# Optimization experiments

Measured on AMD Instinct MI355X. Metric: run time of the kernel, lower is better.

The kernel has to match this reference:

```python
import jax, jax.numpy as jnp
import numpy as np


def setup_inputs() -> dict:
    key = jax.random.key(0)
    k1, k2 = jax.random.split(key)
    N, I, J, K = 256, 32, 32, 256
    x = jax.random.normal(k1, (N, I, K), dtype=jnp.float32)
    z = jax.random.normal(k2, (N, J, K), dtype=jnp.float32)
    return {"x": x, "z": z}


def reference(x, z):
    # Original torch code loops over batch rolls; rolling only permutes the set
    # over which log_softmax (a permutation-invariant logsumexp) is taken, and
    # index 0 of the roll stack is always the diagonal pair (x[n], z[n]).
    # So it is exactly a symmetric InfoNCE over the full pairwise score matrix.
    J = z.shape[1]
    # Full pairwise token-level similarity: [N_x, N_z, I, J]
    sim = jnp.einsum('aik,bjk->abij', x, z)
    # score(x_a, z_b) = sum_{i,j} softmax_i(sim)*sim / J
    w = jax.nn.softmax(sim, axis=2) * sim
    S = w.sum(axis=(2, 3)) / J  # [N_x, N_z]
    diag = jnp.diagonal(S)
    # loss_x[n] = -log_softmax over x-candidates (axis 0) at the diagonal
    loss_x = jax.nn.logsumexp(S, axis=0) - diag
    # loss_z[n] = -log_softmax over z-candidates (axis 1) at the diagonal
    loss_z = jax.nn.logsumexp(S, axis=1) - diag
    loss = loss_x + loss_z
    return loss.mean()  # reduction='mean'
```

## Files before the change

### kernel.cpp

```cpp
#include <hip/hip_runtime.h>
#include <hip/hip_bf16.h>
#include <hip/hip_fp16.h>
#include <stdint.h>


typedef __attribute__((ext_vector_type(8))) short short8;
typedef __attribute__((ext_vector_type(16))) float float16;

#define NTOK 256
#define KDIM 256

__device__ __forceinline__ unsigned short f2bf(float f) {
    unsigned int u = __float_as_uint(f);
    unsigned int r = (u + 0x7fffu + ((u >> 16) & 1u)) >> 16;
    return (unsigned short)r;
}

__device__ __forceinline__ short8 cvt8(const float* p) {
    float4 f0 = ((const float4*)p)[0];
    float4 f1 = ((const float4*)p)[1];
    short8 v;
    v[0] = (short)f2bf(f0.x); v[1] = (short)f2bf(f0.y);
    v[2] = (short)f2bf(f0.z); v[3] = (short)f2bf(f0.w);
    v[4] = (short)f2bf(f1.x); v[5] = (short)f2bf(f1.y);
    v[6] = (short)f2bf(f1.z); v[7] = (short)f2bf(f1.w);
    return v;
}

__global__ void conv_kernel(const float* __restrict__ x,
                            const float* __restrict__ z,
                            short8* __restrict__ outbf,
                            float* __restrict__ out0) {
    const int uid = blockIdx.x * 256 + threadIdx.x;
    if (uid == 0) out0[0] = 0.0f;
    const int u = uid & 262143;
    const float* src = (uid < 262144) ? x : z;
    const int g  = u >> 10;
    const int r  = u & 1023;
    const int ks = r >> 6;
    const int h  = (r >> 5) & 1;
    const int l  = r & 31;
    outbf[uid] = cvt8(src + ((g * 32 + l) * KDIM + ks * 16 + h * 8));
}

__device__ __forceinline__ void tile_epilogue_sp(const float16& c, __half* __restrict__ Sp,
                                                 int a, int b, int lane) {
    float m8[8], m4[4];
#pragma unroll
    for (int r = 0; r < 8; r++) m8[r] = fmaxf(c[2 * r], c[2 * r + 1]);
#pragma unroll
    for (int r = 0; r < 4; r++) m4[r] = fmaxf(m8[2 * r], m8[2 * r + 1]);
    float m = fmaxf(fmaxf(m4[0], m4[1]), fmaxf(m4[2], m4[3]));
    m = fmaxf(m, __shfl_xor(m, 32, 64));

    float s0 = 0.f, s1 = 0.f, s2 = 0.f, s3 = 0.f;
    float w0 = 0.f, w1 = 0.f, w2 = 0.f, w3 = 0.f;
#pragma unroll
    for (int r = 0; r < 16; r += 4) {
        float e0 = __expf(c[r + 0] - m);
        float e1 = __expf(c[r + 1] - m);
        float e2 = __expf(c[r + 2] - m);
        float e3 = __expf(c[r + 3] - m);
        s0 += e0; s1 += e1; s2 += e2; s3 += e3;
        w0 = fmaf(e0, c[r + 0], w0);
        w1 = fmaf(e1, c[r + 1], w1);
        w2 = fmaf(e2, c[r + 2], w2);
        w3 = fmaf(e3, c[r + 3], w3);
    }
    float se  = (s0 + s1) + (s2 + s3);
    float swe = (w0 + w1) + (w2 + w3);
    se  += __shfl_xor(se, 32, 64);
    swe += __shfl_xor(swe, 32, 64);
    float cv = swe * __builtin_amdgcn_rcpf(se);
    Sp[(((a << 8) + b) << 6) + lane] = __float2half_rn(cv);
}

__device__ __forceinline__ void tile_epilogue_bf(const float16& c, float* __restrict__ S,
                                                 int a, int b, int lane) {
    float m8[8], m4[4];
#pragma unroll
    for (int r = 0; r < 8; r++) m8[r] = fmaxf(c[2 * r], c[2 * r + 1]);
#pragma unroll
    for (int r = 0; r < 4; r++) m4[r] = fmaxf(m8[2 * r], m8[2 * r + 1]);
    float m = fmaxf(fmaxf(m4[0], m4[1]), fmaxf(m4[2], m4[3]));
    m = fmaxf(m, __shfl_xor(m, 32, 64));

    float s0 = 0.f, s1 = 0.f, s2 = 0.f, s3 = 0.f;
    float w0 = 0.f, w1 = 0.f, w2 = 0.f, w3 = 0.f;
#pragma unroll
    for (int r = 0; r < 16; r += 4) {
        float e0 = __expf(c[r + 0] - m);
        float e1 = __expf(c[r + 1] - m);
        float e2 = __expf(c[r + 2] - m);
        float e3 = __expf(c[r + 3] - m);
        s0 += e0; s1 += e1; s2 += e2; s3 += e3;
        w0 = fmaf(e0, c[r + 0], w0);
        w1 = fmaf(e1, c[r + 1], w1);
        w2 = fmaf(e2, c[r + 2], w2);
        w3 = fmaf(e3, c[r + 3], w3);
    }
    float se  = (s0 + s1) + (s2 + s3);
    float swe = (w0 + w1) + (w2 + w3);
    se  += __shfl_xor(se, 32, 64);
    swe += __shfl_xor(swe, 32, 64);
    float cv = swe * __builtin_amdgcn_rcpf(se);
#pragma unroll
    for (int off = 1; off < 32; off <<= 1) cv += __shfl_xor(cv, off, 64);
    if (lane == 0) S[a * NTOK + b] = cv * (1.0f / 32.0f);
}

template <bool F32SRC, bool SPSTORE>
__global__ __launch_bounds__(256, 4)
void sim_kernel(const short8* __restrict__ xbf, const short8* __restrict__ zbf,
                const float* __restrict__ xf, const float* __restrict__ zf,
                __half* __restrict__ Sp, float* __restrict__ S) {
    const int tid  = threadIdx.x;
    const int lane = tid & 63;
    const int wid  = tid >> 6;
    const int aw   = wid >> 1;
    const int bw   = wid & 1;
    const int l31  = lane & 31;
    const int half = lane >> 5;
    const int bid  = blockIdx.x;
    const int a0   = (bid >> 6) * 4;
    const int b0   = (bid & 63) * 4;

    const int ag = a0 + 2 * aw;
    const int bg = b0 + 2 * bw;

    const short8* pa = xbf + ag * 1024 + lane;
    const short8* pb = zbf + bg * 1024 + lane;

    const float* fa = xf + ((ag * 32 + l31) * KDIM + half * 8);
    const float* fb = zf + ((bg * 32 + l31) * KDIM + half * 8);

    float16 acc[2][2];
#pragma unroll
    for (int ai = 0; ai < 2; ai++)
#pragma unroll
        for (int bi = 0; bi < 2; bi++)
#pragma unroll
            for (int r = 0; r < 16; r++) acc[ai][bi][r] = 0.0f;

#pragma unroll 4
    for (int ks = 0; ks < 16; ks++) {
        short8 a0f, a1f, b0f, b1f;
        if (F32SRC) {
            a0f = cvt8(fa + ks * 16);
            a1f = cvt8(fa + 32 * KDIM + ks * 16);
            b0f = cvt8(fb + ks * 16);
            b1f = cvt8(fb + 32 * KDIM + ks * 16);
        } else {
            const int off = ks * 64;
            a0f = pa[off];
            a1f = pa[off + 1024];
            b0f = pb[off];
            b1f = pb[off + 1024];
        }
        acc[0][0] = __builtin_amdgcn_mfma_f32_32x32x16_bf16(a0f, b0f, acc[0][0], 0, 0, 0);
        acc[0][1] = __builtin_amdgcn_mfma_f32_32x32x16_bf16(a0f, b1f, acc[0][1], 0, 0, 0);
        acc[1][0] = __builtin_amdgcn_mfma_f32_32x32x16_bf16(a1f, b0f, acc[1][0], 0, 0, 0);
        acc[1][1] = __builtin_amdgcn_mfma_f32_32x32x16_bf16(a1f, b1f, acc[1][1], 0, 0, 0);
    }

#pragma unroll
    for (int ai = 0; ai < 2; ai++)
#pragma unroll
        for (int bi = 0; bi < 2; bi++) {
            if (SPSTORE) tile_epilogue_sp(acc[ai][bi], Sp, ag + ai, bg + bi, lane);
            else         tile_epilogue_bf(acc[ai][bi], S,  ag + ai, bg + bi, lane);
        }
}

__global__ void red_kernel(const __half* __restrict__ Sp, float* __restrict__ S) {
    const int t = blockIdx.x * 256 + threadIdx.x;
    const __half2* h2 = (const __half2*)(Sp + (size_t)t * 64);
    float s = 0.0f;
#pragma unroll
    for (int i = 0; i < 32; i++) {
        float2 f = __half22float2(h2[i]);
        s += f.x + f.y;
    }
    S[t] = s * (1.0f / 64.0f);
}

__global__ void loss_part(const float* __restrict__ S, float* __restrict__ out) {
    const int lane = threadIdx.x & 63;
    const int wid  = threadIdx.x >> 6;
    const int n    = blockIdx.x * 4 + wid;

    float cv[4], rv[4];
#pragma unroll
    for (int k = 0; k < 4; k++) {
        const int t = lane + 64 * k;
        cv[k] = S[t * NTOK + n];
        rv[k] = S[n * NTOK + t];
    }
    float m = fmaxf(fmaxf(cv[0], cv[1]), fmaxf(cv[2], cv[3]));
#pragma unroll
    for (int off = 1; off < 64; off <<= 1) m = fmaxf(m, __shfl_xor(m, off, 64));
    float s = 0.0f;
#pragma unroll
    for (int k = 0; k < 4; k++) s += __expf(cv[k] - m);
#pragma unroll
    for (int off = 1; off < 64; off <<= 1) s += __shfl_xor(s, off, 64);
    float lse_col = m + __logf(s);

    float m2 = fmaxf(fmaxf(rv[0], rv[1]), fmaxf(rv[2], rv[3]));
#pragma unroll
    for (int off = 1; off < 64; off <<= 1) m2 = fmaxf(m2, __shfl_xor(m2, off, 64));
    float s2 = 0.0f;
#pragma unroll
    for (int k = 0; k < 4; k++) s2 += __expf(rv[k] - m2);
#pragma unroll
    for (int off = 1; off < 64; off <<= 1) s2 += __shfl_xor(s2, off, 64);
    float lse_row = m2 + __logf(s2);

    __shared__ float red[4];
    if (lane == 0) {
        float diag = S[n * NTOK + n];
        red[wid] = (lse_col - diag) + (lse_row - diag);
    }
    __syncthreads();
    if (threadIdx.x == 0)
        atomicAdd(out, (red[0] + red[1] + red[2] + red[3]) * (1.0f / 256.0f));
}

__global__ void zero_kernel(float* __restrict__ out) {
    out[0] = 0.0f;
}

extern "C" void kernel_launch(void* const* d_in, const int* in_sizes, int n_in,
                              void* d_out, int out_size, void* d_ws, size_t ws_size,
                              hipStream_t stream) {
    const float* x = (const float*)d_in[0];
    const float* z = (const float*)d_in[1];
    float* out = (float*)d_out;

    const size_t bf_bytes = 524288ull * 16ull;
    const size_t sp_bytes = 65536ull * 64ull * 2ull;
    const size_t s_bytes  = 256ull * 256ull * 4ull;

    if (ws_size >= bf_bytes + sp_bytes + s_bytes) {
        short8* xbf = (short8*)d_ws;
        short8* zbf = xbf + 262144;
        __half* Sp  = (__half*)((char*)d_ws + bf_bytes);
        float*  S   = (float*)((char*)d_ws + bf_bytes + sp_bytes);
        conv_kernel<<<2048, 256, 0, stream>>>(x, z, (short8*)d_ws, out);
        sim_kernel<false, true><<<4096, 256, 0, stream>>>(xbf, zbf, nullptr, nullptr, Sp, S);
        red_kernel<<<256, 256, 0, stream>>>(Sp, S);
        loss_part<<<64, 256, 0, stream>>>(S, out);
    } else if (ws_size >= bf_bytes + s_bytes) {
        short8* xbf = (short8*)d_ws;
        short8* zbf = xbf + 262144;
        float*  S   = (float*)((char*)d_ws + bf_bytes);
        conv_kernel<<<2048, 256, 0, stream>>>(x, z, (short8*)d_ws, out);
        sim_kernel<false, false><<<4096, 256, 0, stream>>>(xbf, zbf, nullptr, nullptr, nullptr, S);
        loss_part<<<64, 256, 0, stream>>>(S, out);
    } else {
        float* S = (float*)d_ws;
        zero_kernel<<<1, 1, 0, stream>>>(out);
        sim_kernel<true, false><<<4096, 256, 0, stream>>>(nullptr, nullptr, x, z, nullptr, S);
        loss_part<<<64, 256, 0, stream>>>(S, out);
    }
}
```

Measured before the change: 120.0 us.

## Stage shared x tiles in LDS and widen per-wave tile to 4x2

Each block now stages four x batch items in LDS via direct global-to-LDS loads and shares them across four waves, each computing a 4x2 tile of batch pairs with register double-buffered z fragments. This halves the grid and raises operand reuse, cutting global/L2 traffic for the x operand. It costs 64KB of LDS per block and more accumulator registers (launch bounds lowered to 2), which reduces occupancy and may expose latency. The epilogue still performs a per-tile softmax that dominates compute.

```diff
diff --git a/kernel.cpp b/kernel.cpp
--- a/kernel.cpp
+++ b/kernel.cpp
@@ -6,6 +6,9 @@
 
 typedef __attribute__((ext_vector_type(8))) short short8;
 typedef __attribute__((ext_vector_type(16))) float float16;
+
+typedef const __attribute__((address_space(1))) unsigned int* gptr_as1;
+typedef __attribute__((address_space(3))) unsigned int* lptr_as3;
 
 #define NTOK 256
 #define KDIM 256
@@ -109,66 +112,90 @@
     if (lane == 0) S[a * NTOK + b] = cv * (1.0f / 32.0f);
 }
 
+#define MFMA_BF16 __builtin_amdgcn_mfma_f32_32x32x16_bf16
+
 template <bool F32SRC, bool SPSTORE>
-__global__ __launch_bounds__(256, 4)
+__global__ __launch_bounds__(256, 2)
 void sim_kernel(const short8* __restrict__ xbf, const short8* __restrict__ zbf,
                 const float* __restrict__ xf, const float* __restrict__ zf,
                 __half* __restrict__ Sp, float* __restrict__ S) {
+    __shared__ short8 sA[4096];
+
     const int tid  = threadIdx.x;
     const int lane = tid & 63;
-    const int wid  = tid >> 6;
-    const int aw   = wid >> 1;
-    const int bw   = wid & 1;
+    const int w    = tid >> 6;
     const int l31  = lane & 31;
     const int half = lane >> 5;
-    const int bid  = blockIdx.x;
-    const int a0   = (bid >> 6) * 4;
-    const int b0   = (bid & 63) * 4;
-
-    const int ag = a0 + 2 * aw;
-    const int bg = b0 + 2 * bw;
-
-    const short8* pa = xbf + ag * 1024 + lane;
-    const short8* pb = zbf + bg * 1024 + lane;
-
-    const float* fa = xf + ((ag * 32 + l31) * KDIM + half * 8);
-    const float* fb = zf + ((bg * 32 + l31) * KDIM + half * 8);
-
-    float16 acc[2][2];
-#pragma unroll
-    for (int ai = 0; ai < 2; ai++)
+
+    const int ablk = blockIdx.x >> 5;
+    const int bblk = blockIdx.x & 31;
+    const int ag0  = ablk * 4;
+    const int bg0  = bblk * 8 + w * 2;
+
+    float16 acc[4][2];
+#pragma unroll
+    for (int ai = 0; ai < 4; ai++)
 #pragma unroll
         for (int bi = 0; bi < 2; bi++)
 #pragma unroll
             for (int r = 0; r < 16; r++) acc[ai][bi][r] = 0.0f;
 
-#pragma unroll 4
-    for (int ks = 0; ks < 16; ks++) {
-        short8 a0f, a1f, b0f, b1f;
-        if (F32SRC) {
-            a0f = cvt8(fa + ks * 16);
-            a1f = cvt8(fa + 32 * KDIM + ks * 16);
-            b0f = cvt8(fb + ks * 16);
-            b1f = cvt8(fb + 32 * KDIM + ks * 16);
-        } else {
-            const int off = ks * 64;
-            a0f = pa[off];
-            a1f = pa[off + 1024];
-            b0f = pb[off];
-            b1f = pb[off + 1024];
-        }
-        acc[0][0] = __builtin_amdgcn_mfma_f32_32x32x16_bf16(a0f, b0f, acc[0][0], 0, 0, 0);
-        acc[0][1] = __builtin_amdgcn_mfma_f32_32x32x16_bf16(a0f, b1f, acc[0][1], 0, 0, 0);
-        acc[1][0] = __builtin_amdgcn_mfma_f32_32x32x16_bf16(a1f, b0f, acc[1][0], 0, 0, 0);
-        acc[1][1] = __builtin_amdgcn_mfma_f32_32x32x16_bf16(a1f, b1f, acc[1][1], 0, 0, 0);
-    }
-
-#pragma unroll
-    for (int ai = 0; ai < 2; ai++)
+    if (!F32SRC) {
+        const short8* asrc = xbf + (size_t)ablk * 4096;
+#pragma unroll
+        for (int i = 0; i < 16; i++) {
+            const short8* g = asrc + i * 256 + w * 64 + lane;
+            short8* l = &sA[i * 256 + w * 64];
+            __builtin_amdgcn_global_load_lds((gptr_as1)g, (lptr_as3)l, 16, 0, 0);
+        }
+        __syncthreads();
+
+        const short8* pb0 = zbf + (bg0 + 0) * 1024 + lane;
+        const short8* pb1 = zbf + (bg0 + 1) * 1024 + lane;
+
+        short8 Ba = pb0[0];
+        short8 Bb = pb1[0];
+#pragma unroll
+        for (int ks = 0; ks < 16; ks++) {
+            short8 Na, Nb;
+            if (ks < 15) { Na = pb0[(ks + 1) * 64]; Nb = pb1[(ks + 1) * 64]; }
+            short8 A0 = sA[ks * 64 + lane];
+            short8 A1 = sA[1024 + ks * 64 + lane];
+            short8 A2 = sA[2048 + ks * 64 + lane];
+            short8 A3 = sA[3072 + ks * 64 + lane];
+            acc[0][0] = MFMA_BF16(A0, Ba, acc[0][0], 0, 0, 0);
+            acc[0][1] = MFMA_BF16(A0, Bb, acc[0][1], 0, 0, 0);
+            acc[1][0] = MFMA_BF16(A1, Ba, acc[1][0], 0, 0, 0);
+            acc[1][1] = MFMA_BF16(A1, Bb, acc[1][1], 0, 0, 0);
+            acc[2][0] = MFMA_BF16(A2, Ba, acc[2][0], 0, 0, 0);
+            acc[2][1] = MFMA_BF16(A2, Bb, acc[2][1], 0, 0, 0);
+            acc[3][0] = MFMA_BF16(A3, Ba, acc[3][0], 0, 0, 0);
+            acc[3][1] = MFMA_BF16(A3, Bb, acc[3][1], 0, 0, 0);
+            Ba = Na; Bb = Nb;
+        }
+    } else {
+        const float* fb0 = zf + (((bg0 + 0) * 32 + l31) * KDIM + half * 8);
+        const float* fb1 = zf + (((bg0 + 1) * 32 + l31) * KDIM + half * 8);
+#pragma unroll 1
+        for (int ks = 0; ks < 16; ks++) {
+            short8 Ba = cvt8(fb0 + ks * 16);
+            short8 Bb = cvt8(fb1 + ks * 16);
+#pragma unroll
+            for (int ai = 0; ai < 4; ai++) {
+                const float* fa = xf + (((ag0 + ai) * 32 + l31) * KDIM + half * 8);
+                short8 Af = cvt8(fa + ks * 16);
+                acc[ai][0] = MFMA_BF16(Af, Ba, acc[ai][0], 0, 0, 0);
+                acc[ai][1] = MFMA_BF16(Af, Bb, acc[ai][1], 0, 0, 0);
+            }
+        }
+    }
+
+#pragma unroll
+    for (int ai = 0; ai < 4; ai++)
 #pragma unroll
         for (int bi = 0; bi < 2; bi++) {
-            if (SPSTORE) tile_epilogue_sp(acc[ai][bi], Sp, ag + ai, bg + bi, lane);
-            else         tile_epilogue_bf(acc[ai][bi], S,  ag + ai, bg + bi, lane);
+            if (SPSTORE) tile_epilogue_sp(acc[ai][bi], Sp, ag0 + ai, bg0 + bi, lane);
+            else         tile_epilogue_bf(acc[ai][bi], S,  ag0 + ai, bg0 + bi, lane);
         }
 }
 
@@ -247,7 +274,7 @@
         __half* Sp  = (__half*)((char*)d_ws + bf_bytes);
         float*  S   = (float*)((char*)d_ws + bf_bytes + sp_bytes);
         conv_kernel<<<2048, 256, 0, stream>>>(x, z, (short8*)d_ws, out);
-        sim_kernel<false, true><<<4096, 256, 0, stream>>>(xbf, zbf, nullptr, nullptr, Sp, S);
+        sim_kernel<false, true><<<2048, 256, 0, stream>>>(xbf, zbf, nullptr, nullptr, Sp, S);
         red_kernel<<<256, 256, 0, stream>>>(Sp, S);
         loss_part<<<64, 256, 0, stream>>>(S, out);
     } else if (ws_size >= bf_bytes + s_bytes) {
@@ -255,12 +282,12 @@
         short8* zbf = xbf + 262144;
         float*  S   = (float*)((char*)d_ws + bf_bytes);
         conv_kernel<<<2048, 256, 0, stream>>>(x, z, (short8*)d_ws, out);
-        sim_kernel<false, false><<<4096, 256, 0, stream>>>(xbf, zbf, nullptr, nullptr, nullptr, S);
+        sim_kernel<false, false><<<2048, 256, 0, stream>>>(xbf, zbf, nullptr, nullptr, nullptr, S);
         loss_part<<<64, 256, 0, stream>>>(S, out);
     } else {
         float* S = (float*)d_ws;
         zero_kernel<<<1, 1, 0, stream>>>(out);
-        sim_kernel<true, false><<<4096, 256, 0, stream>>>(nullptr, nullptr, x, z, nullptr, S);
+        sim_kernel<true, false><<<2048, 256, 0, stream>>>(nullptr, nullptr, x, z, nullptr, S);
         loss_part<<<64, 256, 0, stream>>>(S, out);
     }
 }
```

Measured after the change: 109.7 us. 1.09x faster.
